# Kernel tuning notes

Hardware: AMD Instinct MI355X
Metric: run time of the kernel (lower is better)

Reference implementation:

```python
import jax, jax.numpy as jnp
import numpy as np

D = 256      # model_dim
H = 8        # num_heads
HD = D // H  # head_dim (E)
SIGMA = 1.0
EPS = 1e-5   # LayerNorm eps (torch default)


def setup_inputs() -> dict:
    key = jax.random.key(0)
    ks = jax.random.split(key, 3)
    B, S = 1, 128
    scale = 0.02
    return {
        "inputs": jax.random.normal(ks[0], (B, S, D), jnp.float32),
        "w_in": jax.random.normal(ks[1], (D, D), jnp.float32) * scale,
        "b_in": jnp.zeros((D,), jnp.float32),
        "ln_g": jnp.ones((HD,), jnp.float32),
        "ln_b": jnp.zeros((HD,), jnp.float32),
        "w_out": jax.random.normal(ks[2], (D, D), jnp.float32) * scale,
        "b_out": jnp.zeros((D,), jnp.float32),
    }


def reference(inputs, w_in, b_in, ln_g, ln_b, w_out, b_out):
    B, S, _ = inputs.shape
    # in_project
    x = inputs @ w_in.T + b_in                      # (B,S,D)
    x = x.reshape(B, S, H, HD).transpose(0, 2, 1, 3)  # (B,H,S,HD)
    # LayerNorm over head_dim
    mu = x.mean(-1, keepdims=True)
    var = ((x - mu) ** 2).mean(-1, keepdims=True)
    x = (x - mu) / jnp.sqrt(var + EPS) * ln_g + ln_b
    # Pairwise Gaussian kernel: sum_{e,f} exp(-(x[s,e]-x[t,f])^2 / (2 sigma^2))
    xg = x.reshape(B * H, S, HD)
    diff = xg[:, :, None, :, None] - xg[:, None, :, None, :]  # (BH,S,S,E,E)
    attn = jnp.exp(-(diff * diff) / (2.0 * SIGMA ** 2)).sum((-1, -2)) / HD
    attn = jax.nn.softmax(attn.reshape(B, H, S, S), axis=-1)
    # Dropout omitted (eval mode)
    out = jnp.einsum("bhst,bhtd->bhsd", attn, x)    # (B,H,S,HD)
    out = out.transpose(0, 2, 1, 3).reshape(B, S, D)
    return out @ w_out.T + b_out
```

## Files before the change

kernel.cpp:

```cpp
#include <hip/hip_runtime.h>

#define S_LEN 128
#define DM 256
#define NH 8
#define HD 32

static constexpr float KSCALE     = 0.84932180028801904f;
static constexpr float INV_KSCALE = 1.17741002251547466f;
static constexpr float LOG2E      = 1.44269504088896340f;

__global__ __launch_bounds__(256) void k_proj_ln(
    const float* __restrict__ inp, const float* __restrict__ w_in,
    const float* __restrict__ b_in, const float* __restrict__ ln_g,
    const float* __restrict__ ln_b, float* __restrict__ xn)
{
  const int s = blockIdx.x;
  const int d = threadIdx.x;
  __shared__ float row[DM];
  row[d] = inp[s * DM + d];
  __syncthreads();

  const float4* w4 = reinterpret_cast<const float4*>(w_in + d * DM);
  float acc = b_in[d];
#pragma unroll 8
  for (int k4 = 0; k4 < DM / 4; ++k4) {
    float4 w = w4[k4];
    acc += row[4 * k4 + 0] * w.x + row[4 * k4 + 1] * w.y +
           row[4 * k4 + 2] * w.z + row[4 * k4 + 3] * w.w;
  }

  float sum = acc;
#pragma unroll
  for (int m = 1; m <= 16; m <<= 1) sum += __shfl_xor(sum, m);
  float mu = sum * (1.0f / HD);
  float c = acc - mu;
  float ss = c * c;
#pragma unroll
  for (int m = 1; m <= 16; m <<= 1) ss += __shfl_xor(ss, m);
  float r = rsqrtf(ss * (1.0f / HD) + 1e-5f);

  const int e = d & (HD - 1);
  const int h = d >> 5;
  float y = c * r * ln_g[e] + ln_b[e];
  xn[(h * S_LEN + s) * HD + e] = y * KSCALE;
}

__global__ __launch_bounds__(128) void k_attn(
    const float* __restrict__ xn, float* __restrict__ ah)
{
  const int s = blockIdx.x;
  const int h = blockIdx.y;
  const int t = threadIdx.x;

  __shared__ float xh[S_LEN][HD + 1];
  __shared__ float red[4];
  __shared__ float P[S_LEN];
  __shared__ float po[4][HD];

  const float* base = xn + h * S_LEN * HD;
  for (int i = t; i < S_LEN * HD; i += 128) xh[i >> 5][i & 31] = base[i];
  __syncthreads();

  float xt[HD], xs[HD];
#pragma unroll
  for (int f = 0; f < HD; ++f) xt[f] = xh[t][f];
#pragma unroll
  for (int e = 0; e < HD; ++e) xs[e] = xh[s][e];

  float a0 = 0.f, a1 = 0.f, a2 = 0.f, a3 = 0.f;
  for (int e = 0; e < HD; ++e) {
    const float a = xs[e];
#pragma unroll
    for (int f = 0; f < HD; f += 4) {
      float d0 = a - xt[f + 0]; a0 += __builtin_amdgcn_exp2f(-(d0 * d0));
      float d1 = a - xt[f + 1]; a1 += __builtin_amdgcn_exp2f(-(d1 * d1));
      float d2 = a - xt[f + 2]; a2 += __builtin_amdgcn_exp2f(-(d2 * d2));
      float d3 = a - xt[f + 3]; a3 += __builtin_amdgcn_exp2f(-(d3 * d3));
    }
  }
  const float av = (a0 + a1 + a2 + a3) * (1.0f / HD);

  float m = av;
#pragma unroll
  for (int msk = 1; msk <= 32; msk <<= 1) m = fmaxf(m, __shfl_xor(m, msk));
  if ((t & 63) == 0) red[t >> 6] = m;
  __syncthreads();
  m = fmaxf(red[0], red[1]);

  float p = __builtin_amdgcn_exp2f((av - m) * LOG2E);
  float ssum = p;
#pragma unroll
  for (int msk = 1; msk <= 32; msk <<= 1) ssum += __shfl_xor(ssum, msk);
  if ((t & 63) == 0) red[2 + (t >> 6)] = ssum;
  __syncthreads();
  const float denom = red[2] + red[3];
  P[t] = p / denom;
  __syncthreads();

  const int e = t & 31, g = t >> 5;
  float o = 0.f;
#pragma unroll
  for (int i = 0; i < 32; ++i) {
    const int tt = g * 32 + i;
    o += P[tt] * xh[tt][e];
  }
  po[g][e] = o;
  __syncthreads();
  if (t < HD) {
    float out = (po[0][t] + po[1][t] + po[2][t] + po[3][t]) * INV_KSCALE;
    ah[(h * S_LEN + s) * HD + t] = out;
  }
}

__global__ __launch_bounds__(256) void k_out(
    const float* __restrict__ ah, const float* __restrict__ w_out,
    const float* __restrict__ b_out, float* __restrict__ out)
{
  const int s = blockIdx.x;
  const int d = threadIdx.x;
  __shared__ float row[DM];
  const int h = d >> 5, e = d & 31;
  row[d] = ah[(h * S_LEN + s) * HD + e];
  __syncthreads();

  const float4* w4 = reinterpret_cast<const float4*>(w_out + d * DM);
  float acc = b_out[d];
#pragma unroll 8
  for (int k4 = 0; k4 < DM / 4; ++k4) {
    float4 w = w4[k4];
    acc += row[4 * k4 + 0] * w.x + row[4 * k4 + 1] * w.y +
           row[4 * k4 + 2] * w.z + row[4 * k4 + 3] * w.w;
  }
  out[s * DM + d] = acc;
}

extern "C" void kernel_launch(void* const* d_in, const int* in_sizes, int n_in,
                              void* d_out, int out_size, void* d_ws, size_t ws_size,
                              hipStream_t stream) {
  const float* inp   = (const float*)d_in[0];
  const float* w_in  = (const float*)d_in[1];
  const float* b_in  = (const float*)d_in[2];
  const float* ln_g  = (const float*)d_in[3];
  const float* ln_b  = (const float*)d_in[4];
  const float* w_out = (const float*)d_in[5];
  const float* b_out = (const float*)d_in[6];
  float* out = (float*)d_out;

  float* xn = (float*)d_ws;
  float* ah = xn + S_LEN * DM;

  k_proj_ln<<<S_LEN, DM, 0, stream>>>(inp, w_in, b_in, ln_g, ln_b, xn);
  k_attn<<<dim3(S_LEN, NH), 128, 0, stream>>>(xn, ah);
  k_out<<<S_LEN, DM, 0, stream>>>(ah, w_out, b_out, out);
}
```

Measured before the change: 42.65 us.

## Replace pairwise Gaussian kernel with truncated Taylor feature expansion and fuse attention with output projection

Measured after the change: 40.03 us. -6.2%, faster.

```diff
diff --git a/kernel.cpp b/kernel.cpp
--- a/kernel.cpp
+++ b/kernel.cpp
@@ -4,134 +4,173 @@
 #define DM 256
 #define NH 8
 #define HD 32
+#define NP 56
 
-static constexpr float KSCALE     = 0.84932180028801904f;
-static constexpr float INV_KSCALE = 1.17741002251547466f;
-static constexpr float LOG2E      = 1.44269504088896340f;
+static constexpr float LOG2E    = 1.44269504088896340f;
+static constexpr float HLOG2E   = 0.72134752044448170f;
 
-__global__ __launch_bounds__(256) void k_proj_ln(
+__device__ const float RS[NP] = {
+  0.0f,        1.0f,        0.70710678f, 0.57735027f, 0.5f,        0.44721360f,
+  0.40824829f, 0.37796447f, 0.35355339f, 0.33333333f, 0.31622777f, 0.30151134f,
+  0.28867513f, 0.27735010f, 0.26726124f, 0.25819889f, 0.25f,       0.24253563f,
+  0.23570226f, 0.22941573f, 0.22360680f, 0.21821789f, 0.21320072f, 0.20851441f,
+  0.20412415f, 0.2f,        0.19611614f, 0.19245009f, 0.18898224f, 0.18569534f,
+  0.18257419f, 0.17960530f, 0.17677670f, 0.17407766f, 0.17149859f, 0.16903085f,
+  0.16666667f, 0.16439899f, 0.16222142f, 0.16012815f, 0.15811388f, 0.15617376f,
+  0.15430335f, 0.15249857f, 0.15075567f, 0.14907120f, 0.14744196f, 0.14586499f,
+  0.14433757f, 0.14285714f, 0.14142136f, 0.14002801f, 0.13867505f, 0.13736056f,
+  0.13608276f, 0.13483997f
+};
+
+__global__ __launch_bounds__(128) void k_proj_ln_feat(
     const float* __restrict__ inp, const float* __restrict__ w_in,
     const float* __restrict__ b_in, const float* __restrict__ ln_g,
-    const float* __restrict__ ln_b, float* __restrict__ xn)
+    const float* __restrict__ ln_b, float* __restrict__ xn,
+    float* __restrict__ F, float* __restrict__ Fs)
 {
-  const int s = blockIdx.x;
-  const int d = threadIdx.x;
+  const int s     = blockIdx.x >> 1;
+  const int half  = blockIdx.x & 1;
+  const int dbase = half * 128;
+  const int tid   = threadIdx.x;
+
   __shared__ float row[DM];
-  row[d] = inp[s * DM + d];
+  __shared__ float xblk[128];
+
+  row[tid]       = inp[s * DM + tid];
+  row[tid + 128] = inp[s * DM + tid + 128];
   __syncthreads();
 
-  const float4* w4 = reinterpret_cast<const float4*>(w_in + d * DM);
-  float acc = b_in[d];
-#pragma unroll 8
-  for (int k4 = 0; k4 < DM / 4; ++k4) {
-    float4 w = w4[k4];
-    acc += row[4 * k4 + 0] * w.x + row[4 * k4 + 1] * w.y +
-           row[4 * k4 + 2] * w.z + row[4 * k4 + 3] * w.w;
+  const int g = tid >> 4;
+  const int j = tid & 15;
+  const float4* rowv = reinterpret_cast<const float4*>(row);
+  for (int p = 0; p < 16; ++p) {
+    const int dl = p * 8 + g;
+    const int d  = dbase + dl;
+    const float4* w4 = reinterpret_cast<const float4*>(w_in + d * DM);
+    float4 a4 = {0.f, 0.f, 0.f, 0.f};
+#pragma unroll
+    for (int c = 0; c < 4; ++c) {
+      float4 w = w4[c * 16 + j];
+      float4 r = rowv[c * 16 + j];
+      a4.x += w.x * r.x; a4.y += w.y * r.y; a4.z += w.z * r.z; a4.w += w.w * r.w;
+    }
+    float acc = (a4.x + a4.y) + (a4.z + a4.w);
+#pragma unroll
+    for (int m = 1; m <= 8; m <<= 1) acc += __shfl_xor(acc, m);
+    if (j == 0) xblk[dl] = acc + b_in[d];
   }
+  __syncthreads();
 
-  float sum = acc;
+  const float accd = xblk[tid];
+  float sum = accd;
 #pragma unroll
   for (int m = 1; m <= 16; m <<= 1) sum += __shfl_xor(sum, m);
-  float mu = sum * (1.0f / HD);
-  float c = acc - mu;
+  const float mu = sum * (1.0f / HD);
+  const float c  = accd - mu;
   float ss = c * c;
 #pragma unroll
   for (int m = 1; m <= 16; m <<= 1) ss += __shfl_xor(ss, m);
-  float r = rsqrtf(ss * (1.0f / HD) + 1e-5f);
+  const float r = rsqrtf(ss * (1.0f / HD) + 1e-5f);
 
-  const int e = d & (HD - 1);
-  const int h = d >> 5;
-  float y = c * r * ln_g[e] + ln_b[e];
-  xn[(h * S_LEN + s) * HD + e] = y * KSCALE;
-}
+  const int e = tid & 31;
+  const int h = half * 4 + (tid >> 5);
+  const float y = c * r * ln_g[e] + ln_b[e];
+  xn[(h * S_LEN + s) * HD + e] = y;
 
-__global__ __launch_bounds__(128) void k_attn(
-    const float* __restrict__ xn, float* __restrict__ ah)
-{
-  const int s = blockIdx.x;
-  const int h = blockIdx.y;
-  const int t = threadIdx.x;
-
-  __shared__ float xh[S_LEN][HD + 1];
-  __shared__ float red[4];
-  __shared__ float P[S_LEN];
-  __shared__ float po[4][HD];
-
-  const float* base = xn + h * S_LEN * HD;
-  for (int i = t; i < S_LEN * HD; i += 128) xh[i >> 5][i & 31] = base[i];
-  __syncthreads();
-
-  float xt[HD], xs[HD];
+  float psi = __builtin_amdgcn_exp2f(-HLOG2E * y * y);
+  {
+    float u = psi;
 #pragma unroll
-  for (int f = 0; f < HD; ++f) xt[f] = xh[t][f];
+    for (int m = 1; m <= 16; m <<= 1) u += __shfl_xor(u, m);
+    if (e == 0) { F[(h * NP) * S_LEN + s] = u; Fs[s * (NH * NP) + h * NP] = u; }
+  }
+  for (int n = 1; n < NP; ++n) {
+    psi *= y * RS[n];
+    float u = psi;
 #pragma unroll
-  for (int e = 0; e < HD; ++e) xs[e] = xh[s][e];
-
-  float a0 = 0.f, a1 = 0.f, a2 = 0.f, a3 = 0.f;
-  for (int e = 0; e < HD; ++e) {
-    const float a = xs[e];
-#pragma unroll
-    for (int f = 0; f < HD; f += 4) {
-      float d0 = a - xt[f + 0]; a0 += __builtin_amdgcn_exp2f(-(d0 * d0));
-      float d1 = a - xt[f + 1]; a1 += __builtin_amdgcn_exp2f(-(d1 * d1));
-      float d2 = a - xt[f + 2]; a2 += __builtin_amdgcn_exp2f(-(d2 * d2));
-      float d3 = a - xt[f + 3]; a3 += __builtin_amdgcn_exp2f(-(d3 * d3));
-    }
-  }
-  const float av = (a0 + a1 + a2 + a3) * (1.0f / HD);
-
-  float m = av;
-#pragma unroll
-  for (int msk = 1; msk <= 32; msk <<= 1) m = fmaxf(m, __shfl_xor(m, msk));
-  if ((t & 63) == 0) red[t >> 6] = m;
-  __syncthreads();
-  m = fmaxf(red[0], red[1]);
-
-  float p = __builtin_amdgcn_exp2f((av - m) * LOG2E);
-  float ssum = p;
-#pragma unroll
-  for (int msk = 1; msk <= 32; msk <<= 1) ssum += __shfl_xor(ssum, msk);
-  if ((t & 63) == 0) red[2 + (t >> 6)] = ssum;
-  __syncthreads();
-  const float denom = red[2] + red[3];
-  P[t] = p / denom;
-  __syncthreads();
-
-  const int e = t & 31, g = t >> 5;
-  float o = 0.f;
-#pragma unroll
-  for (int i = 0; i < 32; ++i) {
-    const int tt = g * 32 + i;
-    o += P[tt] * xh[tt][e];
-  }
-  po[g][e] = o;
-  __syncthreads();
-  if (t < HD) {
-    float out = (po[0][t] + po[1][t] + po[2][t] + po[3][t]) * INV_KSCALE;
-    ah[(h * S_LEN + s) * HD + t] = out;
+    for (int m = 1; m <= 16; m <<= 1) u += __shfl_xor(u, m);
+    if (e == 0) { F[(h * NP + n) * S_LEN + s] = u; Fs[s * (NH * NP) + h * NP + n] = u; }
   }
 }
 
-__global__ __launch_bounds__(256) void k_out(
-    const float* __restrict__ ah, const float* __restrict__ w_out,
+__global__ __launch_bounds__(256) void k_attn_out(
+    const float* __restrict__ xn, const float* __restrict__ F,
+    const float* __restrict__ Fs, const float* __restrict__ w_out,
     const float* __restrict__ b_out, float* __restrict__ out)
 {
-  const int s = blockIdx.x;
-  const int d = threadIdx.x;
-  __shared__ float row[DM];
-  const int h = d >> 5, e = d & 31;
-  row[d] = ah[(h * S_LEN + s) * HD + e];
+  const int s   = blockIdx.x;
+  const int tid = threadIdx.x;
+
+  __shared__ float fsl[NH * NP];
+  __shared__ float Pl[NH][S_LEN];
+  __shared__ float ahrow[DM];
+
+  if (tid < 224) {
+    fsl[tid]       = Fs[s * (NH * NP) + tid];
+    fsl[tid + 224] = Fs[s * (NH * NP) + tid + 224];
+  }
   __syncthreads();
 
-  const float4* w4 = reinterpret_cast<const float4*>(w_out + d * DM);
-  float acc = b_out[d];
+  {
+    const int h = tid >> 5;
+    const int l = tid & 31;
+    const float4* Fh4 = reinterpret_cast<const float4*>(F + h * NP * S_LEN);
+    const float*  fr  = fsl + h * NP;
+    float4 acc = {0.f, 0.f, 0.f, 0.f};
 #pragma unroll 8
-  for (int k4 = 0; k4 < DM / 4; ++k4) {
-    float4 w = w4[k4];
-    acc += row[4 * k4 + 0] * w.x + row[4 * k4 + 1] * w.y +
-           row[4 * k4 + 2] * w.z + row[4 * k4 + 3] * w.w;
+    for (int n = 0; n < NP; ++n) {
+      const float un = fr[n];
+      float4 v = Fh4[n * 32 + l];
+      acc.x += un * v.x; acc.y += un * v.y; acc.z += un * v.z; acc.w += un * v.w;
+    }
+    const float sc = 1.0f / HD;
+    float r0 = acc.x * sc, r1 = acc.y * sc, r2 = acc.z * sc, r3 = acc.w * sc;
+    float m = fmaxf(fmaxf(r0, r1), fmaxf(r2, r3));
+#pragma unroll
+    for (int msk = 1; msk <= 16; msk <<= 1) m = fmaxf(m, __shfl_xor(m, msk));
+    float p0 = __builtin_amdgcn_exp2f((r0 - m) * LOG2E);
+    float p1 = __builtin_amdgcn_exp2f((r1 - m) * LOG2E);
+    float p2 = __builtin_amdgcn_exp2f((r2 - m) * LOG2E);
+    float p3 = __builtin_amdgcn_exp2f((r3 - m) * LOG2E);
+    float ps = (p0 + p1) + (p2 + p3);
+#pragma unroll
+    for (int msk = 1; msk <= 16; msk <<= 1) ps += __shfl_xor(ps, msk);
+    const float inv = 1.0f / ps;
+    float4 pv = {p0 * inv, p1 * inv, p2 * inv, p3 * inv};
+    *reinterpret_cast<float4*>(&Pl[h][4 * l]) = pv;
   }
-  out[s * DM + d] = acc;
+  __syncthreads();
+
+  {
+    const int h = tid >> 5;
+    const int e = tid & 31;
+    const float* xh = xn + h * S_LEN * HD + e;
+    const float* Ph = Pl[h];
+    float o = 0.f;
+#pragma unroll 8
+    for (int t = 0; t < S_LEN; ++t) o += Ph[t] * xh[t * HD];
+    ahrow[h * HD + e] = o;
+  }
+  __syncthreads();
+
+  const int g = tid >> 4;
+  const int j = tid & 15;
+  const float4* rowv = reinterpret_cast<const float4*>(ahrow);
+  for (int p = 0; p < 16; ++p) {
+    const int d = p * 16 + g;
+    const float4* w4 = reinterpret_cast<const float4*>(w_out + d * DM);
+    float4 a4 = {0.f, 0.f, 0.f, 0.f};
+#pragma unroll
+    for (int c = 0; c < 4; ++c) {
+      float4 w = w4[c * 16 + j];
+      float4 r = rowv[c * 16 + j];
+      a4.x += w.x * r.x; a4.y += w.y * r.y; a4.z += w.z * r.z; a4.w += w.w * r.w;
+    }
+    float acc = (a4.x + a4.y) + (a4.z + a4.w);
+#pragma unroll
+    for (int m = 1; m <= 8; m <<= 1) acc += __shfl_xor(acc, m);
+    if (j == 0) out[s * DM + d] = acc + b_out[d];
+  }
 }
 
 extern "C" void kernel_launch(void* const* d_in, const int* in_sizes, int n_in,
@@ -147,9 +186,9 @@
   float* out = (float*)d_out;
 
   float* xn = (float*)d_ws;
-  float* ah = xn + S_LEN * DM;
+  float* F  = xn + NH * S_LEN * HD;
+  float* Fs = F + NH * NP * S_LEN;
 
-  k_proj_ln<<<S_LEN, DM, 0, stream>>>(inp, w_in, b_in, ln_g, ln_b, xn);
-  k_attn<<<dim3(S_LEN, NH), 128, 0, stream>>>(xn, ah);
-  k_out<<<S_LEN, DM, 0, stream>>>(ah, w_out, b_out, out);
+  k_proj_ln_feat<<<2 * S_LEN, 128, 0, stream>>>(inp, w_in, b_in, ln_g, ln_b, xn, F, Fs);
+  k_attn_out<<<S_LEN, 256, 0, stream>>>(xn, F, Fs, w_out, b_out, out);
 }
```
